# Kernel tuning notes

Hardware: AMD Instinct MI355X
Metric: run time of the kernel (lower is better)

## Reference

```python
import jax, jax.numpy as jnp
import numpy as np

C = 256
EPS = 1e-5

def setup_inputs() -> dict:
    key = jax.random.key(0)
    ks = jax.random.split(key, 10)
    N, H, W = 4, 64, 64
    Ch = C // 2
    sc = 1.0 / np.sqrt(C)
    sch = 1.0 / np.sqrt(Ch)
    return {
        "x": jax.random.normal(ks[0], (N, C, H, W), dtype=jnp.float32),
        "cfc": jax.random.normal(ks[1], (C, 2), dtype=jnp.float32) * 0.1,
        "theta_w": jax.random.normal(ks[2], (Ch, C), dtype=jnp.float32) * sc,
        "theta_b": jax.random.normal(ks[3], (Ch,), dtype=jnp.float32) * 0.01,
        "phi_w": jax.random.normal(ks[4], (Ch, C), dtype=jnp.float32) * sc,
        "phi_b": jax.random.normal(ks[5], (Ch,), dtype=jnp.float32) * 0.01,
        "g_w": jax.random.normal(ks[6], (Ch, C), dtype=jnp.float32) * sc,
        "g_b": jax.random.normal(ks[7], (Ch,), dtype=jnp.float32) * 0.01,
        "out_w": jax.random.normal(ks[8], (C, Ch), dtype=jnp.float32) * sch,
        "out_b": jax.random.normal(ks[9], (C,), dtype=jnp.float32) * 0.01,
    }

def reference(x, cfc, theta_w, theta_b, phi_w, phi_b, g_w, g_b, out_w, out_b):
    N, Cc, H, W = x.shape
    L = H * W
    xf = x.reshape(N, Cc, L)
    # SRM style pooling: per-channel mean and (unbiased) std over spatial dims
    mean = jnp.mean(xf, axis=2)                              # [N,C]
    var = jnp.var(xf, axis=2, ddof=1) + EPS                  # torch .var() is unbiased
    std = jnp.sqrt(var)
    # style integration: z = mean*cfc[:,0] + std*cfc[:,1], gate = sigmoid(z)
    z = mean * cfc[None, :, 0] + std * cfc[None, :, 1]       # [N,C]
    gate = jax.nn.sigmoid(z)[:, :, None]                     # [N,C,1]
    s = xf * gate                                            # srm_out flattened [N,C,L]
    # 1x1 convs == per-pixel linear maps
    theta = jnp.einsum('oc,ncl->nol', theta_w, s) + theta_b[None, :, None]  # [N,C/2,L]
    phi = jnp.einsum('oc,ncl->nol', phi_w, s) + phi_b[None, :, None]
    g = jnp.einsum('oc,ncl->nol', g_w, s) + g_b[None, :, None]
    # attention[n,i,j] = sum_c theta[n,c,i]*phi[n,c,j]; softmax over j (no 1/sqrt(d))
    attn = jax.nn.softmax(jnp.einsum('nci,ncj->nij', theta, phi), axis=-1)  # [N,L,L]
    # nl_out[n,c,i] = sum_j g[n,c,j]*attn[n,i,j]
    nl = jnp.einsum('ncj,nij->nci', g, attn)                 # [N,C/2,L]
    nl = jnp.einsum('oc,ncl->nol', out_w, nl) + out_b[None, :, None]        # [N,C,L]
    out = s + nl
    return out.reshape(N, Cc, H, W)
```

## Files before the change

kernel.cpp:

```cpp
#include <hip/hip_runtime.h>
#include <hip/hip_bf16.h>

#define LSP 4096
#define NC  256
#define NH  128
#define KB  64
#define QW  64
#define SPLIT 4
#define NTILE ((LSP / SPLIT) / KB)

typedef __attribute__((ext_vector_type(8))) short short8;
typedef __attribute__((ext_vector_type(4))) float f32x4;
typedef __attribute__((ext_vector_type(4))) unsigned int u32x4;
typedef __attribute__((ext_vector_type(2))) unsigned int u32x2;
typedef __hip_bfloat16 bf16;

#define MFMA16(a,b,c) __builtin_amdgcn_mfma_f32_16x16x32_bf16((a),(b),(c),0,0,0)

typedef __attribute__((address_space(1))) const void gas_t;
typedef __attribute__((address_space(3))) void las_t;
#define GLDS16(g, l) __builtin_amdgcn_global_load_lds((gas_t*)(g), (las_t*)(l), 16, 0, 0)

static __device__ __forceinline__ unsigned short f2bf(float f) {
  bf16 h = __float2bfloat16(f);
  return __builtin_bit_cast(unsigned short, h);
}
static __device__ __forceinline__ unsigned int packbf2(float a, float b) {
  return (unsigned int)f2bf(a) | ((unsigned int)f2bf(b) << 16);
}
static __device__ __forceinline__ float bf2f(unsigned short u) {
  return __builtin_bit_cast(float, (unsigned int)u << 16);
}

__global__ __launch_bounds__(256) void k_pre(const float* __restrict__ a0,
    const float* __restrict__ a1, const float* __restrict__ a2,
    const float* __restrict__ a3, const float* __restrict__ tb,
    const float* __restrict__ pb, bf16* __restrict__ dst, float* __restrict__ bcat,
    const float* __restrict__ x, const float* __restrict__ cfc,
    float* __restrict__ gate) {
  int b = blockIdx.x;
  if (b < 512) {
    int i = b * 256 + threadIdx.x;
    int seg = i >> 15, off = i & 32767;
    const float* s = (seg == 0) ? a0 : (seg == 1) ? a1 : (seg == 2) ? a2 : a3;
    dst[i] = __float2bfloat16(s[off]);
    if (b == 0)
      bcat[threadIdx.x] = threadIdx.x < 128 ? tb[threadIdx.x] : pb[threadIdx.x - 128];
    return;
  }
  int nc = b - 512;
  const float4* x4 = (const float4*)(x + (size_t)nc * LSP);
  float s = 0.f, q = 0.f;
  for (int i = threadIdx.x; i < LSP / 4; i += 256) {
    float4 v = x4[i];
    s += v.x + v.y + v.z + v.w;
    q += v.x * v.x + v.y * v.y + v.z * v.z + v.w * v.w;
  }
#pragma unroll
  for (int o = 32; o > 0; o >>= 1) { s += __shfl_xor(s, o); q += __shfl_xor(q, o); }
  __shared__ float rs[4], rq[4];
  int w = threadIdx.x >> 6;
  if ((threadIdx.x & 63) == 0) { rs[w] = s; rq[w] = q; }
  __syncthreads();
  if (threadIdx.x == 0) {
    float S = rs[0] + rs[1] + rs[2] + rs[3];
    float Q = rq[0] + rq[1] + rq[2] + rq[3];
    float mean = S / (float)LSP;
    float var = (Q - S * S / (float)LSP) / (float)(LSP - 1) + 1e-5f;
    float sd = sqrtf(var);
    int c = nc & (NC - 1);
    float z = mean * cfc[2 * c] + sd * cfc[2 * c + 1];
    gate[nc] = 1.f / (1.f + __expf(-z));
  }
}

__global__ __launch_bounds__(256) void k_scale_t(const float* __restrict__ x,
    const float* __restrict__ gate, bf16* __restrict__ s_t) {
  int n = blockIdx.z;
  int c0 = blockIdx.y * 32;
  int l = blockIdx.x * 256 + threadIdx.x;
  unsigned int pk[16];
#pragma unroll
  for (int i = 0; i < 32; i += 2) {
    int c = c0 + i;
    float g0 = gate[n * NC + c];
    float g1 = gate[n * NC + c + 1];
    float v0 = x[((size_t)(n * NC + c)) * LSP + l] * g0;
    float v1 = x[((size_t)(n * NC + c + 1)) * LSP + l] * g1;
    pk[i >> 1] = packbf2(v0, v1);
  }
  u32x4* dst = (u32x4*)(s_t + ((size_t)n * LSP + l) * NC + c0);
#pragma unroll
  for (int k = 0; k < 4; ++k) dst[k] = ((const u32x4*)pk)[k];
}

static __device__ __forceinline__ void gemm_nt_body(const bf16* __restrict__ A,
    const bf16* __restrict__ B, const float* __restrict__ bias, int bias_row,
    bf16* __restrict__ D, int Nd, int Kd, int bx) {
  int tn = Nd >> 6;
  int m0 = (bx / tn) * 64, n0 = (bx % tn) * 64;
  int tid = threadIdx.x, w = tid >> 6, lane = tid & 63;
  int lo = lane & 15, g = lane >> 4;
  f32x4 zero = {0.f, 0.f, 0.f, 0.f};
  f32x4 acc[4];
#pragma unroll
  for (int i = 0; i < 4; ++i) acc[i] = zero;
  for (int kc = 0; kc < Kd; kc += 32) {
    short8 bfr = *(const short8*)(B + (size_t)(n0 + w * 16 + lo) * Kd + kc + g * 8);
#pragma unroll
    for (int i = 0; i < 4; ++i) {
      short8 afr = *(const short8*)(A + (size_t)(m0 + 16 * i + lo) * Kd + kc + g * 8);
      acc[i] = MFMA16(afr, bfr, acc[i]);
    }
  }
  int col = n0 + w * 16 + lo;
#pragma unroll
  for (int i = 0; i < 4; ++i)
#pragma unroll
    for (int r = 0; r < 4; ++r) {
      int row = m0 + 16 * i + g * 4 + r;
      float bv = bias_row ? bias[row] : bias[col];
      D[(size_t)row * Nd + col] = __float2bfloat16(acc[i][r] + bv);
    }
}

__global__ __launch_bounds__(256) void k_gemms(const bf16* __restrict__ s_t,
    const bf16* __restrict__ wbf, const float* __restrict__ bcat,
    const float* __restrict__ g_b, bf16* __restrict__ thph, bf16* __restrict__ gTb) {
  int z = blockIdx.z, bx = blockIdx.x;
  if (bx < 256) {
    gemm_nt_body(s_t + (size_t)z * LSP * NC, wbf, bcat, 0,
                 thph + (size_t)z * LSP * 256, 256, NC, bx);
  } else {
    gemm_nt_body(wbf + 65536, s_t + (size_t)z * LSP * NC, g_b, 1,
                 gTb + (size_t)z * NH * LSP, LSP, NC, bx - 256);
  }
}

__global__ __launch_bounds__(256, 1) void k_attn(const bf16* __restrict__ thph,
    const bf16* __restrict__ gT, bf16* __restrict__ Opart, float* __restrict__ ml) {
  __shared__ bf16 Kl[3][KB * NH];
  __shared__ bf16 Vl[3][NH * KB];
  __shared__ bf16 Pl[4][QW * KB];

  const int n = blockIdx.z, sp = blockIdx.y;
  const int tid = threadIdx.x, w = tid >> 6, lane = tid & 63;
  const int lo = lane & 15, g = lane >> 4;
  const int swz = (lo & 7) << 4;

  const bf16* thn = thph + (size_t)n * LSP * 256;
  const bf16* gv  = gT + (size_t)n * NH * LSP;
  const int q0 = blockIdx.x * 256 + w * QW;
  const int j0base = sp * (LSP / SPLIT);

  short8 qf[4][4];
#pragma unroll
  for (int qs = 0; qs < 4; ++qs)
#pragma unroll
    for (int kc = 0; kc < 4; ++kc)
      qf[qs][kc] = *(const short8*)(thn + (size_t)(q0 + qs * 16 + lo) * 256 + kc * 32 + g * 8);

  size_t koff[4], voff[4];
  int ldso[4];
#pragma unroll
  for (int i = 0; i < 4; ++i) {
    int ci = i * 256 + tid;
    int kj = ci >> 4, kcc = ci & 15;
    koff[i] = (size_t)kj * 256 + 128 + ((kcc ^ (kj & 7)) * 8);
    int vd = ci >> 3, vc2 = ci & 7;
    voff[i] = (size_t)vd * LSP + ((vc2 ^ (vd & 7)) * 8);
    ldso[i] = ci * 16;
  }

#define STAGE(JT, BUF) do { \
    const bf16* ksrc = thn + (size_t)(j0base + (JT) * KB) * 256; \
    const bf16* vsrc = gv + (j0base + (JT) * KB); \
    char* kdst = (char*)&Kl[BUF][0]; \
    char* vdst = (char*)&Vl[BUF][0]; \
    _Pragma("unroll") \
    for (int i = 0; i < 4; ++i) { \
      GLDS16(ksrc + koff[i], kdst + ldso[i]); \
      GLDS16(vsrc + voff[i], vdst + ldso[i]); \
    } } while (0)

  f32x4 zero = {0.f, 0.f, 0.f, 0.f};
  f32x4 acc[4][8];
#pragma unroll
  for (int qs = 0; qs < 4; ++qs)
#pragma unroll
    for (int dc = 0; dc < 8; ++dc) acc[qs][dc] = zero;
  float mv[4] = {-1e30f, -1e30f, -1e30f, -1e30f};
  float ls[4] = {0.f, 0.f, 0.f, 0.f};

  STAGE(0, 0);
  STAGE(1, 1);

  char* pwb = (char*)&Pl[w][0];

  for (int t = 0; t < NTILE; ++t) {
    int cur = t % 3;
    if (t < NTILE - 1) asm volatile("s_waitcnt vmcnt(8)" ::: "memory");
    else               asm volatile("s_waitcnt vmcnt(0)" ::: "memory");
    __builtin_amdgcn_sched_barrier(0);
    __builtin_amdgcn_s_barrier();
    if (t + 2 < NTILE) STAGE(t + 2, (t + 2) % 3);

    const char* Kb = (const char*)&Kl[cur][0];
    const char* Vb = (const char*)&Vl[cur][0];

    short8 kfr[4][4];
#pragma unroll
    for (int jt = 0; jt < 4; ++jt)
#pragma unroll
      for (int kc = 0; kc < 4; ++kc)
        kfr[jt][kc] = *(const short8*)(Kb + (jt * 16 + lo) * 256 + ((kc * 64 + g * 16) ^ swz));

#pragma unroll
    for (int qs = 0; qs < 4; ++qs) {
      f32x4 st[4];
#pragma unroll
      for (int jt = 0; jt < 4; ++jt) st[jt] = zero;
#pragma unroll
      for (int kc = 0; kc < 4; ++kc)
#pragma unroll
        for (int jt = 0; jt < 4; ++jt)
          st[jt] = MFMA16(kfr[jt][kc], qf[qs][kc], st[jt]);

      float t0 = fmaxf(fmaxf(st[0][0], st[0][1]), fmaxf(st[0][2], st[0][3]));
      float t1 = fmaxf(fmaxf(st[1][0], st[1][1]), fmaxf(st[1][2], st[1][3]));
      float t2 = fmaxf(fmaxf(st[2][0], st[2][1]), fmaxf(st[2][2], st[2][3]));
      float t3 = fmaxf(fmaxf(st[3][0], st[3][1]), fmaxf(st[3][2], st[3][3]));
      float tq = fmaxf(fmaxf(t0, t1), fmaxf(t2, t3));
      tq = fmaxf(tq, __shfl_xor(tq, 16));
      tq = fmaxf(tq, __shfl_xor(tq, 32));

      if (__any(tq > mv[qs] + 8.f)) {
        float nm = fmaxf(mv[qs], tq);
        float a = __expf(mv[qs] - nm);
        mv[qs] = nm; ls[qs] *= a;
#pragma unroll
        for (int r = 0; r < 4; ++r) {
          float b = __shfl(a, g * 4 + r);
#pragma unroll
          for (int dc = 0; dc < 8; ++dc) acc[qs][dc][r] *= b;
        }
      }

      float mm = mv[qs], psum = 0.f;
      int rowb = (qs * 16 + lo) * 128;
#pragma unroll
      for (int jt = 0; jt < 4; ++jt) {
        float e0 = __expf(st[jt][0] - mm);
        float e1 = __expf(st[jt][1] - mm);
        float e2 = __expf(st[jt][2] - mm);
        float e3 = __expf(st[jt][3] - mm);
        psum += (e0 + e1) + (e2 + e3);
        u32x2 pk;
        pk.x = packbf2(e0, e1);
        pk.y = packbf2(e2, e3);
        *(u32x2*)(pwb + rowb + ((jt * 32 + g * 8) ^ swz)) = pk;
      }
      psum += __shfl_xor(psum, 16);
      psum += __shfl_xor(psum, 32);
      ls[qs] += psum;
    }

    asm volatile("" ::: "memory");
#pragma unroll
    for (int kc2 = 0; kc2 < 2; ++kc2) {
      int kbb = kc2 * 64 + g * 16;
      short8 pa[4];
#pragma unroll
      for (int qs = 0; qs < 4; ++qs)
        pa[qs] = *(const short8*)(pwb + (qs * 16 + lo) * 128 + (kbb ^ swz));
#pragma unroll
      for (int dc = 0; dc < 8; ++dc) {
        int d = dc * 16 + lo;
        short8 vb = *(const short8*)(Vb + d * 128 + (kbb ^ ((d & 7) << 4)));
#pragma unroll
        for (int qs = 0; qs < 4; ++qs)
          acc[qs][dc] = MFMA16(pa[qs], vb, acc[qs][dc]);
      }
    }
  }

  bf16* opb = Opart + ((size_t)(sp * 4 + n) * LSP + q0) * NH;
#pragma unroll
  for (int qs = 0; qs < 4; ++qs)
#pragma unroll
    for (int dc = 0; dc < 8; ++dc)
#pragma unroll
      for (int r = 0; r < 4; ++r)
        opb[(size_t)(qs * 16 + g * 4 + r) * NH + dc * 16 + lo] =
            __float2bfloat16(acc[qs][dc][r]);
  if (g == 0) {
    float2* mlp = (float2*)ml + (size_t)(sp * 4 + n) * LSP + q0;
#pragma unroll
    for (int qs = 0; qs < 4; ++qs)
      mlp[qs * 16 + lo] = make_float2(mv[qs], ls[qs]);
  }
#undef STAGE
}

__global__ __launch_bounds__(256) void k_final(const bf16* __restrict__ Wo,
    const bf16* __restrict__ Opart, const float* __restrict__ ml,
    const float* __restrict__ x, const float* __restrict__ gate,
    const float* __restrict__ ob, float* __restrict__ out) {
  int n = blockIdx.z;
  int m0 = (blockIdx.x >> 6) * 64, n0 = (blockIdx.x & 63) * 64;
  int tid = threadIdx.x, w = tid >> 6, lane = tid & 63;
  int lo = lane & 15, g = lane >> 4;
  int col = n0 + w * 16 + lo;

  float sc[SPLIT];
  {
    float2 m4[SPLIT];
    float mx = -1e30f;
#pragma unroll
    for (int s = 0; s < SPLIT; ++s) {
      m4[s] = ((const float2*)ml)[(size_t)(s * 4 + n) * LSP + col];
      mx = fmaxf(mx, m4[s].x);
    }
    float den = 0.f;
#pragma unroll
    for (int s = 0; s < SPLIT; ++s) { sc[s] = __expf(m4[s].x - mx); den += m4[s].y * sc[s]; }
    float inv = 1.f / den;
#pragma unroll
    for (int s = 0; s < SPLIT; ++s) sc[s] *= inv;
  }

  f32x4 zero = {0.f, 0.f, 0.f, 0.f};
  f32x4 acc[4];
#pragma unroll
  for (int i = 0; i < 4; ++i) acc[i] = zero;
#pragma unroll
  for (int kc = 0; kc < 4; ++kc) {
    float bv[8] = {0.f, 0.f, 0.f, 0.f, 0.f, 0.f, 0.f, 0.f};
#pragma unroll
    for (int s = 0; s < SPLIT; ++s) {
      short8 v = *(const short8*)(Opart + ((size_t)(s * 4 + n) * LSP + col) * NH + kc * 32 + g * 8);
#pragma unroll
      for (int e = 0; e < 8; ++e)
        bv[e] += sc[s] * bf2f((unsigned short)v[e]);
    }
    u32x4 pk4;
    pk4.x = packbf2(bv[0], bv[1]); pk4.y = packbf2(bv[2], bv[3]);
    pk4.z = packbf2(bv[4], bv[5]); pk4.w = packbf2(bv[6], bv[7]);
    short8 bfr = __builtin_bit_cast(short8, pk4);
#pragma unroll
    for (int i = 0; i < 4; ++i) {
      short8 afr = *(const short8*)(Wo + (size_t)(m0 + 16 * i + lo) * NH + kc * 32 + g * 8);
      acc[i] = MFMA16(afr, bfr, acc[i]);
    }
  }
#pragma unroll
  for (int i = 0; i < 4; ++i)
#pragma unroll
    for (int r = 0; r < 4; ++r) {
      int c = m0 + 16 * i + g * 4 + r;
      size_t xo = ((size_t)(n * NC + c)) * LSP + col;
      out[xo] = acc[i][r] + ob[c] + x[xo] * gate[n * NC + c];
    }
}

extern "C" void kernel_launch(void* const* d_in, const int* in_sizes, int n_in,
                              void* d_out, int out_size, void* d_ws, size_t ws_size,
                              hipStream_t stream) {
  const float* x       = (const float*)d_in[0];
  const float* cfc     = (const float*)d_in[1];
  const float* theta_w = (const float*)d_in[2];
  const float* theta_b = (const float*)d_in[3];
  const float* phi_w   = (const float*)d_in[4];
  const float* phi_b   = (const float*)d_in[5];
  const float* g_w     = (const float*)d_in[6];
  const float* g_b     = (const float*)d_in[7];
  const float* out_w   = (const float*)d_in[8];
  const float* out_b   = (const float*)d_in[9];
  float* out = (float*)d_out;

  char* p = (char*)d_ws;
  auto alloc = [&](size_t bytes) { char* r = p; p += (bytes + 255) & ~(size_t)255; return r; };
  float* gate  = (float*)alloc(4 * NC * sizeof(float));
  bf16* s_t    = (bf16*)alloc((size_t)4 * LSP * NC * 2);
  bf16* thph   = (bf16*)alloc((size_t)4 * LSP * 256 * 2);
  bf16* gTb    = (bf16*)alloc((size_t)4 * NH * LSP * 2);
  bf16* wbf    = (bf16*)alloc((size_t)4 * 32768 * 2);
  float* bcat  = (float*)alloc(256 * sizeof(float));
  bf16* Opart  = (bf16*)alloc((size_t)SPLIT * 4 * LSP * NH * 2);
  float* ml    = (float*)alloc((size_t)SPLIT * 4 * LSP * 2 * 4);

  k_pre<<<1536, 256, 0, stream>>>(theta_w, phi_w, g_w, out_w, theta_b, phi_b,
                                  wbf, bcat, x, cfc, gate);
  k_scale_t<<<dim3(16, 8, 4), 256, 0, stream>>>(x, gate, s_t);
  k_gemms<<<dim3(384, 1, 4), 256, 0, stream>>>(s_t, wbf, bcat, g_b, thph, gTb);
  k_attn<<<dim3(LSP / 256, SPLIT, 4), 256, 0, stream>>>(thph, gTb, Opart, ml);
  k_final<<<dim3(256, 1, 4), 256, 0, stream>>>(wbf + 98304, Opart, ml, x, gate, out_b, out);
}
```

Measured before the change: 213.0 us.

## Use 8 waves per attention block and transpose scale via LDS

```diff
diff --git a/kernel.cpp b/kernel.cpp
--- a/kernel.cpp
+++ b/kernel.cpp
@@ -5,7 +5,7 @@
 #define NC  256
 #define NH  128
 #define KB  64
-#define QW  64
+#define QW  32
 #define SPLIT 4
 #define NTILE ((LSP / SPLIT) / KB)
 
@@ -30,6 +30,9 @@
 }
 static __device__ __forceinline__ float bf2f(unsigned short u) {
   return __builtin_bit_cast(float, (unsigned int)u << 16);
+}
+static __device__ __forceinline__ unsigned short bfu(bf16 h) {
+  return __builtin_bit_cast(unsigned short, h);
 }
 
 __global__ __launch_bounds__(256) void k_pre(const float* __restrict__ a0,
@@ -76,22 +79,32 @@
 
 __global__ __launch_bounds__(256) void k_scale_t(const float* __restrict__ x,
     const float* __restrict__ gate, bf16* __restrict__ s_t) {
+  __shared__ bf16 T[64][66];
   int n = blockIdx.z;
-  int c0 = blockIdx.y * 32;
-  int l = blockIdx.x * 256 + threadIdx.x;
-  unsigned int pk[16];
-#pragma unroll
-  for (int i = 0; i < 32; i += 2) {
-    int c = c0 + i;
-    float g0 = gate[n * NC + c];
-    float g1 = gate[n * NC + c + 1];
-    float v0 = x[((size_t)(n * NC + c)) * LSP + l] * g0;
-    float v1 = x[((size_t)(n * NC + c + 1)) * LSP + l] * g1;
-    pk[i >> 1] = packbf2(v0, v1);
-  }
-  u32x4* dst = (u32x4*)(s_t + ((size_t)n * LSP + l) * NC + c0);
-#pragma unroll
-  for (int k = 0; k < 4; ++k) dst[k] = ((const u32x4*)pk)[k];
+  int c0 = blockIdx.y * 64;
+  int l0 = blockIdx.x * 64;
+  int tid = threadIdx.x;
+  int lr = tid & 63, cr = tid >> 6;
+#pragma unroll
+  for (int k = 0; k < 16; ++k) {
+    int c = cr * 16 + k;
+    float gv = gate[n * NC + c0 + c];
+    float v = x[((size_t)(n * NC + c0 + c)) * LSP + l0 + lr] * gv;
+    T[c][lr] = __float2bfloat16(v);
+  }
+  __syncthreads();
+  int cg = tid & 7, lw = tid >> 3;
+#pragma unroll
+  for (int ps = 0; ps < 2; ++ps) {
+    int l = lw + ps * 32;
+    unsigned int pk[4];
+#pragma unroll
+    for (int e = 0; e < 4; ++e)
+      pk[e] = (unsigned int)bfu(T[cg * 8 + 2 * e][l]) |
+              ((unsigned int)bfu(T[cg * 8 + 2 * e + 1][l]) << 16);
+    *(u32x4*)(s_t + ((size_t)n * LSP + l0 + l) * NC + c0 + cg * 8) =
+        *(const u32x4*)pk;
+  }
 }
 
 static __device__ __forceinline__ void gemm_nt_body(const bf16* __restrict__ A,
@@ -137,11 +150,11 @@
   }
 }
 
-__global__ __launch_bounds__(256, 1) void k_attn(const bf16* __restrict__ thph,
+__global__ __launch_bounds__(512, 2) void k_attn(const bf16* __restrict__ thph,
     const bf16* __restrict__ gT, bf16* __restrict__ Opart, float* __restrict__ ml) {
   __shared__ bf16 Kl[3][KB * NH];
   __shared__ bf16 Vl[3][NH * KB];
-  __shared__ bf16 Pl[4][QW * KB];
+  __shared__ bf16 Pl[8][QW * KB];
 
   const int n = blockIdx.z, sp = blockIdx.y;
   const int tid = threadIdx.x, w = tid >> 6, lane = tid & 63;
@@ -153,18 +166,18 @@
   const int q0 = blockIdx.x * 256 + w * QW;
   const int j0base = sp * (LSP / SPLIT);
 
-  short8 qf[4][4];
-#pragma unroll
-  for (int qs = 0; qs < 4; ++qs)
+  short8 qf[2][4];
+#pragma unroll
+  for (int qs = 0; qs < 2; ++qs)
 #pragma unroll
     for (int kc = 0; kc < 4; ++kc)
       qf[qs][kc] = *(const short8*)(thn + (size_t)(q0 + qs * 16 + lo) * 256 + kc * 32 + g * 8);
 
-  size_t koff[4], voff[4];
-  int ldso[4];
-#pragma unroll
-  for (int i = 0; i < 4; ++i) {
-    int ci = i * 256 + tid;
+  size_t koff[2], voff[2];
+  int ldso[2];
+#pragma unroll
+  for (int i = 0; i < 2; ++i) {
+    int ci = i * 512 + tid;
     int kj = ci >> 4, kcc = ci & 15;
     koff[i] = (size_t)kj * 256 + 128 + ((kcc ^ (kj & 7)) * 8);
     int vd = ci >> 3, vc2 = ci & 7;
@@ -178,19 +191,19 @@
     char* kdst = (char*)&Kl[BUF][0]; \
     char* vdst = (char*)&Vl[BUF][0]; \
     _Pragma("unroll") \
-    for (int i = 0; i < 4; ++i) { \
+    for (int i = 0; i < 2; ++i) { \
       GLDS16(ksrc + koff[i], kdst + ldso[i]); \
       GLDS16(vsrc + voff[i], vdst + ldso[i]); \
     } } while (0)
 
   f32x4 zero = {0.f, 0.f, 0.f, 0.f};
-  f32x4 acc[4][8];
-#pragma unroll
-  for (int qs = 0; qs < 4; ++qs)
+  f32x4 acc[2][8];
+#pragma unroll
+  for (int qs = 0; qs < 2; ++qs)
 #pragma unroll
     for (int dc = 0; dc < 8; ++dc) acc[qs][dc] = zero;
-  float mv[4] = {-1e30f, -1e30f, -1e30f, -1e30f};
-  float ls[4] = {0.f, 0.f, 0.f, 0.f};
+  float mv[2] = {-1e30f, -1e30f};
+  float ls[2] = {0.f, 0.f};
 
   STAGE(0, 0);
   STAGE(1, 1);
@@ -199,10 +212,11 @@
 
   for (int t = 0; t < NTILE; ++t) {
     int cur = t % 3;
-    if (t < NTILE - 1) asm volatile("s_waitcnt vmcnt(8)" ::: "memory");
+    if (t < NTILE - 1) asm volatile("s_waitcnt vmcnt(4)" ::: "memory");
     else               asm volatile("s_waitcnt vmcnt(0)" ::: "memory");
     __builtin_amdgcn_sched_barrier(0);
     __builtin_amdgcn_s_barrier();
+    __builtin_amdgcn_sched_barrier(0);
     if (t + 2 < NTILE) STAGE(t + 2, (t + 2) % 3);
 
     const char* Kb = (const char*)&Kl[cur][0];
@@ -215,21 +229,27 @@
       for (int kc = 0; kc < 4; ++kc)
         kfr[jt][kc] = *(const short8*)(Kb + (jt * 16 + lo) * 256 + ((kc * 64 + g * 16) ^ swz));
 
-#pragma unroll
-    for (int qs = 0; qs < 4; ++qs) {
-      f32x4 st[4];
-#pragma unroll
-      for (int jt = 0; jt < 4; ++jt) st[jt] = zero;
-#pragma unroll
-      for (int kc = 0; kc < 4; ++kc)
-#pragma unroll
-        for (int jt = 0; jt < 4; ++jt)
-          st[jt] = MFMA16(kfr[jt][kc], qf[qs][kc], st[jt]);
-
-      float t0 = fmaxf(fmaxf(st[0][0], st[0][1]), fmaxf(st[0][2], st[0][3]));
-      float t1 = fmaxf(fmaxf(st[1][0], st[1][1]), fmaxf(st[1][2], st[1][3]));
-      float t2 = fmaxf(fmaxf(st[2][0], st[2][1]), fmaxf(st[2][2], st[2][3]));
-      float t3 = fmaxf(fmaxf(st[3][0], st[3][1]), fmaxf(st[3][2], st[3][3]));
+    f32x4 st[2][4];
+#pragma unroll
+    for (int qs = 0; qs < 2; ++qs)
+#pragma unroll
+      for (int jt = 0; jt < 4; ++jt) st[qs][jt] = zero;
+    __builtin_amdgcn_s_setprio(1);
+#pragma unroll
+    for (int kc = 0; kc < 4; ++kc)
+#pragma unroll
+      for (int jt = 0; jt < 4; ++jt) {
+        st[0][jt] = MFMA16(kfr[jt][kc], qf[0][kc], st[0][jt]);
+        st[1][jt] = MFMA16(kfr[jt][kc], qf[1][kc], st[1][jt]);
+      }
+    __builtin_amdgcn_s_setprio(0);
+
+#pragma unroll
+    for (int qs = 0; qs < 2; ++qs) {
+      float t0 = fmaxf(fmaxf(st[qs][0][0], st[qs][0][1]), fmaxf(st[qs][0][2], st[qs][0][3]));
+      float t1 = fmaxf(fmaxf(st[qs][1][0], st[qs][1][1]), fmaxf(st[qs][1][2], st[qs][1][3]));
+      float t2 = fmaxf(fmaxf(st[qs][2][0], st[qs][2][1]), fmaxf(st[qs][2][2], st[qs][2][3]));
+      float t3 = fmaxf(fmaxf(st[qs][3][0], st[qs][3][1]), fmaxf(st[qs][3][2], st[qs][3][3]));
       float tq = fmaxf(fmaxf(t0, t1), fmaxf(t2, t3));
       tq = fmaxf(tq, __shfl_xor(tq, 16));
       tq = fmaxf(tq, __shfl_xor(tq, 32));
@@ -250,10 +270,10 @@
       int rowb = (qs * 16 + lo) * 128;
 #pragma unroll
       for (int jt = 0; jt < 4; ++jt) {
-        float e0 = __expf(st[jt][0] - mm);
-        float e1 = __expf(st[jt][1] - mm);
-        float e2 = __expf(st[jt][2] - mm);
-        float e3 = __expf(st[jt][3] - mm);
+        float e0 = __expf(st[qs][jt][0] - mm);
+        float e1 = __expf(st[qs][jt][1] - mm);
+        float e2 = __expf(st[qs][jt][2] - mm);
+        float e3 = __expf(st[qs][jt][3] - mm);
         psum += (e0 + e1) + (e2 + e3);
         u32x2 pk;
         pk.x = packbf2(e0, e1);
@@ -269,24 +289,23 @@
 #pragma unroll
     for (int kc2 = 0; kc2 < 2; ++kc2) {
       int kbb = kc2 * 64 + g * 16;
-      short8 pa[4];
-#pragma unroll
-      for (int qs = 0; qs < 4; ++qs)
-        pa[qs] = *(const short8*)(pwb + (qs * 16 + lo) * 128 + (kbb ^ swz));
+      short8 pa0 = *(const short8*)(pwb + lo * 128 + (kbb ^ swz));
+      short8 pa1 = *(const short8*)(pwb + (16 + lo) * 128 + (kbb ^ swz));
+      __builtin_amdgcn_s_setprio(1);
 #pragma unroll
       for (int dc = 0; dc < 8; ++dc) {
         int d = dc * 16 + lo;
         short8 vb = *(const short8*)(Vb + d * 128 + (kbb ^ ((d & 7) << 4)));
-#pragma unroll
-        for (int qs = 0; qs < 4; ++qs)
-          acc[qs][dc] = MFMA16(pa[qs], vb, acc[qs][dc]);
+        acc[0][dc] = MFMA16(pa0, vb, acc[0][dc]);
+        acc[1][dc] = MFMA16(pa1, vb, acc[1][dc]);
       }
+      __builtin_amdgcn_s_setprio(0);
     }
   }
 
   bf16* opb = Opart + ((size_t)(sp * 4 + n) * LSP + q0) * NH;
 #pragma unroll
-  for (int qs = 0; qs < 4; ++qs)
+  for (int qs = 0; qs < 2; ++qs)
 #pragma unroll
     for (int dc = 0; dc < 8; ++dc)
 #pragma unroll
@@ -296,7 +315,7 @@
   if (g == 0) {
     float2* mlp = (float2*)ml + (size_t)(sp * 4 + n) * LSP + q0;
 #pragma unroll
-    for (int qs = 0; qs < 4; ++qs)
+    for (int qs = 0; qs < 2; ++qs)
       mlp[qs * 16 + lo] = make_float2(mv[qs], ls[qs]);
   }
 #undef STAGE
@@ -391,8 +410,8 @@
 
   k_pre<<<1536, 256, 0, stream>>>(theta_w, phi_w, g_w, out_w, theta_b, phi_b,
                                   wbf, bcat, x, cfc, gate);
-  k_scale_t<<<dim3(16, 8, 4), 256, 0, stream>>>(x, gate, s_t);
+  k_scale_t<<<dim3(64, 4, 4), 256, 0, stream>>>(x, gate, s_t);
   k_gemms<<<dim3(384, 1, 4), 256, 0, stream>>>(s_t, wbf, bcat, g_b, thph, gTb);
-  k_attn<<<dim3(LSP / 256, SPLIT, 4), 256, 0, stream>>>(thph, gTb, Opart, ml);
+  k_attn<<<dim3(LSP / 256, SPLIT, 4), 512, 0, stream>>>(thph, gTb, Opart, ml);
   k_final<<<dim3(256, 1, 4), 256, 0, stream>>>(wbf + 98304, Opart, ml, x, gate, out_b, out);
 }
```

Measured after the change: 197.4 us. 1.08x faster.
